# Kernel tuning notes

Hardware: AMD Instinct MI355X
Metric: run time of the kernel (lower is better)

Reference implementation:

```python
import jax, jax.numpy as jnp
import numpy as np

VOCAB = 32000
NUM_NEW = 512
HIDDEN = 4096
PROF_DIM = 64
MLP_HID = 256
B, S = 4, 4096


def setup_inputs() -> dict:
    key = jax.random.key(0)
    ks = jax.random.split(key, 8)
    return {
        "input_ids": jax.random.randint(ks[0], (B, S), 0, VOCAB + NUM_NEW),
        "emb_weight": jax.random.normal(ks[1], (VOCAB + NUM_NEW, HIDDEN), jnp.float32) * 0.02,
        "tool_semantics": jax.random.normal(ks[2], (NUM_NEW, HIDDEN), jnp.float32) * 0.02,
        "profiles": jax.random.normal(ks[3], (NUM_NEW, PROF_DIM), jnp.float32),
        "W1": jax.random.normal(ks[4], (PROF_DIM, MLP_HID), jnp.float32) * (1.0 / np.sqrt(PROF_DIM)),
        "b1": jnp.zeros((MLP_HID,), jnp.float32),
        "W2": jax.random.normal(ks[5], (MLP_HID, HIDDEN), jnp.float32) * (1.0 / np.sqrt(MLP_HID)),
        "b2": jnp.zeros((HIDDEN,), jnp.float32),
        "new_token_start_idx": VOCAB,
    }


def reference(input_ids, emb_weight, tool_semantics, profiles, W1, b1, W2, b2, new_token_start_idx):
    # Base embedding lookup: [B, S, H]
    base = emb_weight[input_ids]
    is_new = input_ids >= new_token_start_idx  # [B, S] bool
    # Clip relative indices so gathers are always in-range (masked out elsewhere)
    rel = jnp.clip(input_ids - new_token_start_idx, 0, tool_semantics.shape[0] - 1)
    sem = tool_semantics[rel]          # [B, S, H]
    prof = profiles[rel]               # [B, S, P]
    # Profile encoder MLP (hypernetwork): P -> MLP_HID -> H
    h = jax.nn.relu(jnp.einsum("bsp,ph->bsh", prof, W1) + b1)
    delta = jnp.einsum("bsh,hd->bsd", h, W2) + b2
    # Token_Embedding = semantics + profile delta for tool tokens, else base
    return jnp.where(is_new[..., None], sem + delta, base)
```

## Files before the change

### kernel.cpp

```cpp
#include <hip/hip_runtime.h>
#include <hip/hip_bf16.h>

constexpr int VOCAB    = 32000;
constexpr int NUM_NEW  = 512;
constexpr int HIDDEN   = 4096;
constexpr int PROF_DIM = 64;
constexpr int MLP_HID  = 256;

constexpr int TOK_PER_BLK  = 8;
constexpr int COLS_PER_BLK = 512;

typedef float f32x4 __attribute__((ext_vector_type(4)));

__global__ __launch_bounds__(256) void build_combined_kernel(
    const float* __restrict__ tool_semantics,
    const float* __restrict__ profiles,
    const float* __restrict__ W1,
    const float* __restrict__ b1,
    const float* __restrict__ W2,
    const float* __restrict__ b2,
    float* __restrict__ combined)
{
    __shared__ float prof_s[TOK_PER_BLK][PROF_DIM];
    __shared__ float h_s[TOK_PER_BLK][MLP_HID];

    const int t    = threadIdx.x;
    const int tok0 = blockIdx.y * TOK_PER_BLK;
    const int col0 = blockIdx.x * COLS_PER_BLK;

    for (int i = t; i < TOK_PER_BLK * PROF_DIM; i += 256) {
        const int tok = i / PROF_DIM;
        const int p   = i % PROF_DIM;
        prof_s[tok][p] = profiles[(tok0 + tok) * PROF_DIM + p];
    }
    __syncthreads();

    {
        float acc[TOK_PER_BLK];
        const float bias = b1[t];
#pragma unroll
        for (int tok = 0; tok < TOK_PER_BLK; ++tok) acc[tok] = bias;
        for (int p = 0; p < PROF_DIM; ++p) {
            const float w = W1[p * MLP_HID + t];
#pragma unroll
            for (int tok = 0; tok < TOK_PER_BLK; ++tok)
                acc[tok] = fmaf(prof_s[tok][p], w, acc[tok]);
        }
#pragma unroll
        for (int tok = 0; tok < TOK_PER_BLK; ++tok)
            h_s[tok][t] = fmaxf(acc[tok], 0.0f);
    }
    __syncthreads();

    const int c = col0 + t * 2;
    float2 acc2[TOK_PER_BLK];
#pragma unroll
    for (int tok = 0; tok < TOK_PER_BLK; ++tok) acc2[tok] = make_float2(0.f, 0.f);

    for (int k = 0; k < MLP_HID; ++k) {
        const float2 w2 = *(const float2*)&W2[k * HIDDEN + c];
#pragma unroll
        for (int tok = 0; tok < TOK_PER_BLK; ++tok) {
            const float hv = h_s[tok][k];
            acc2[tok].x = fmaf(hv, w2.x, acc2[tok].x);
            acc2[tok].y = fmaf(hv, w2.y, acc2[tok].y);
        }
    }

    const float2 bias2 = *(const float2*)&b2[c];
#pragma unroll
    for (int tok = 0; tok < TOK_PER_BLK; ++tok) {
        const float2 sem = *(const float2*)&tool_semantics[(size_t)(tok0 + tok) * HIDDEN + c];
        float2 r;
        r.x = sem.x + acc2[tok].x + bias2.x;
        r.y = sem.y + acc2[tok].y + bias2.y;
        *(float2*)&combined[(size_t)(tok0 + tok) * HIDDEN + c] = r;
    }
}

__global__ __launch_bounds__(256) void gather_rows_kernel(
    const int* __restrict__ input_ids,
    const float* __restrict__ emb_weight,
    const float* __restrict__ combined,
    const int* __restrict__ new_start_ptr,
    float* __restrict__ out)
{
    const int row       = blockIdx.x;
    const int id        = input_ids[row];
    const int new_start = *new_start_ptr;

    const float* src;
    if (id >= new_start) {
        int rel = id - new_start;
        if (rel > NUM_NEW - 1) rel = NUM_NEW - 1;
        src = combined + (size_t)rel * HIDDEN;
    } else {
        src = emb_weight + (size_t)id * HIDDEN;
    }

    const f32x4* s = (const f32x4*)src;
    f32x4*       d = (f32x4*)(out + (size_t)row * HIDDEN);
    const int t = threadIdx.x;

    f32x4 v0 = s[t];
    f32x4 v1 = s[t + 256];
    f32x4 v2 = s[t + 512];
    f32x4 v3 = s[t + 768];
    __builtin_nontemporal_store(v0, d + t);
    __builtin_nontemporal_store(v1, d + t + 256);
    __builtin_nontemporal_store(v2, d + t + 512);
    __builtin_nontemporal_store(v3, d + t + 768);
}

extern "C" void kernel_launch(void* const* d_in, const int* in_sizes, int n_in,
                              void* d_out, int out_size, void* d_ws, size_t ws_size,
                              hipStream_t stream) {
    const int*   input_ids      = (const int*)d_in[0];
    const float* emb_weight     = (const float*)d_in[1];
    const float* tool_semantics = (const float*)d_in[2];
    const float* profiles       = (const float*)d_in[3];
    const float* W1             = (const float*)d_in[4];
    const float* b1             = (const float*)d_in[5];
    const float* W2             = (const float*)d_in[6];
    const float* b2             = (const float*)d_in[7];
    const int*   new_start_ptr  = (const int*)d_in[8];
    float*       out            = (float*)d_out;

    const int num_rows = in_sizes[0];

    float* combined = (float*)d_ws;

    dim3 gridA(HIDDEN / COLS_PER_BLK, NUM_NEW / TOK_PER_BLK);
    build_combined_kernel<<<gridA, 256, 0, stream>>>(
        tool_semantics, profiles, W1, b1, W2, b2, combined);

    gather_rows_kernel<<<num_rows, 256, 0, stream>>>(
        input_ids, emb_weight, combined, new_start_ptr, out);
}
```

Measured before the change: 770.6 us.

## Fuse tool-token MLP into per-row gather, dropping precomputed combined table

Replaces the two-kernel scheme, which precomputed a 512-row combined table and then gathered from it, with a single kernel. Each row block either copies its base embedding row or runs the profile MLP for that one token. This removes a launch and the workspace round trip. In exchange, every tool token recomputes the full 256x4096 W2 product. With random ids about 1.6% of 16384 rows (~250 rows) are tool tokens, so W2 is read about 250 times instead of once per 8 tokens, and those blocks become long serial tails.

Result: slower. 821.2 us (+6.6%).

```diff
diff --git a/kernel.cpp b/kernel.cpp
--- a/kernel.cpp
+++ b/kernel.cpp
@@ -7,109 +7,84 @@
 constexpr int PROF_DIM = 64;
 constexpr int MLP_HID  = 256;
 
-constexpr int TOK_PER_BLK  = 8;
-constexpr int COLS_PER_BLK = 512;
-
 typedef float f32x4 __attribute__((ext_vector_type(4)));
 
-__global__ __launch_bounds__(256) void build_combined_kernel(
+__global__ __launch_bounds__(256) void fused_embed_kernel(
+    const int*   __restrict__ input_ids,
+    const float* __restrict__ emb_weight,
     const float* __restrict__ tool_semantics,
     const float* __restrict__ profiles,
     const float* __restrict__ W1,
     const float* __restrict__ b1,
     const float* __restrict__ W2,
     const float* __restrict__ b2,
-    float* __restrict__ combined)
+    const int*   __restrict__ new_start_ptr,
+    float*       __restrict__ out)
 {
-    __shared__ float prof_s[TOK_PER_BLK][PROF_DIM];
-    __shared__ float h_s[TOK_PER_BLK][MLP_HID];
+    __shared__ float prof_s[PROF_DIM];
+    __shared__ float h_s[MLP_HID];
 
-    const int t    = threadIdx.x;
-    const int tok0 = blockIdx.y * TOK_PER_BLK;
-    const int col0 = blockIdx.x * COLS_PER_BLK;
+    const int row       = blockIdx.x;
+    const int t         = threadIdx.x;
+    const int id        = input_ids[row];
+    const int new_start = *new_start_ptr;
 
-    for (int i = t; i < TOK_PER_BLK * PROF_DIM; i += 256) {
-        const int tok = i / PROF_DIM;
-        const int p   = i % PROF_DIM;
-        prof_s[tok][p] = profiles[(tok0 + tok) * PROF_DIM + p];
+    f32x4* d = (f32x4*)(out + (size_t)row * HIDDEN);
+
+    if (id < new_start) {
+        const f32x4* s = (const f32x4*)(emb_weight + (size_t)id * HIDDEN);
+        f32x4 v0 = s[t];
+        f32x4 v1 = s[t + 256];
+        f32x4 v2 = s[t + 512];
+        f32x4 v3 = s[t + 768];
+        __builtin_nontemporal_store(v0, d + t);
+        __builtin_nontemporal_store(v1, d + t + 256);
+        __builtin_nontemporal_store(v2, d + t + 512);
+        __builtin_nontemporal_store(v3, d + t + 768);
+        return;
+    }
+
+    int rel = id - new_start;
+    if (rel > NUM_NEW - 1) rel = NUM_NEW - 1;
+
+    if (t < PROF_DIM) prof_s[t] = profiles[rel * PROF_DIM + t];
+    __syncthreads();
+
+    {
+        float acc = b1[t];
+#pragma unroll
+        for (int p = 0; p < PROF_DIM; ++p)
+            acc = fmaf(prof_s[p], W1[p * MLP_HID + t], acc);
+        h_s[t] = fmaxf(acc, 0.0f);
     }
     __syncthreads();
 
-    {
-        float acc[TOK_PER_BLK];
-        const float bias = b1[t];
-#pragma unroll
-        for (int tok = 0; tok < TOK_PER_BLK; ++tok) acc[tok] = bias;
-        for (int p = 0; p < PROF_DIM; ++p) {
-            const float w = W1[p * MLP_HID + t];
-#pragma unroll
-            for (int tok = 0; tok < TOK_PER_BLK; ++tok)
-                acc[tok] = fmaf(prof_s[tok][p], w, acc[tok]);
-        }
-#pragma unroll
-        for (int tok = 0; tok < TOK_PER_BLK; ++tok)
-            h_s[tok][t] = fmaxf(acc[tok], 0.0f);
-    }
-    __syncthreads();
+    const f32x4* sem4 = (const f32x4*)(tool_semantics + (size_t)rel * HIDDEN);
+    const f32x4* b2_4 = (const f32x4*)b2;
+    const f32x4* W2_4 = (const f32x4*)W2;
 
-    const int c = col0 + t * 2;
-    float2 acc2[TOK_PER_BLK];
-#pragma unroll
-    for (int tok = 0; tok < TOK_PER_BLK; ++tok) acc2[tok] = make_float2(0.f, 0.f);
+    f32x4 acc0 = sem4[t]       + b2_4[t];
+    f32x4 acc1 = sem4[t + 256] + b2_4[t + 256];
+    f32x4 acc2 = sem4[t + 512] + b2_4[t + 512];
+    f32x4 acc3 = sem4[t + 768] + b2_4[t + 768];
 
     for (int k = 0; k < MLP_HID; ++k) {
-        const float2 w2 = *(const float2*)&W2[k * HIDDEN + c];
-#pragma unroll
-        for (int tok = 0; tok < TOK_PER_BLK; ++tok) {
-            const float hv = h_s[tok][k];
-            acc2[tok].x = fmaf(hv, w2.x, acc2[tok].x);
-            acc2[tok].y = fmaf(hv, w2.y, acc2[tok].y);
-        }
+        const float hv = h_s[k];
+        const f32x4* w2row = W2_4 + (size_t)k * (HIDDEN / 4);
+        const f32x4 w0 = w2row[t];
+        const f32x4 w1 = w2row[t + 256];
+        const f32x4 w2v = w2row[t + 512];
+        const f32x4 w3 = w2row[t + 768];
+        acc0 += hv * w0;
+        acc1 += hv * w1;
+        acc2 += hv * w2v;
+        acc3 += hv * w3;
     }
 
-    const float2 bias2 = *(const float2*)&b2[c];
-#pragma unroll
-    for (int tok = 0; tok < TOK_PER_BLK; ++tok) {
-        const float2 sem = *(const float2*)&tool_semantics[(size_t)(tok0 + tok) * HIDDEN + c];
-        float2 r;
-        r.x = sem.x + acc2[tok].x + bias2.x;
-        r.y = sem.y + acc2[tok].y + bias2.y;
-        *(float2*)&combined[(size_t)(tok0 + tok) * HIDDEN + c] = r;
-    }
-}
-
-__global__ __launch_bounds__(256) void gather_rows_kernel(
-    const int* __restrict__ input_ids,
-    const float* __restrict__ emb_weight,
-    const float* __restrict__ combined,
-    const int* __restrict__ new_start_ptr,
-    float* __restrict__ out)
-{
-    const int row       = blockIdx.x;
-    const int id        = input_ids[row];
-    const int new_start = *new_start_ptr;
-
-    const float* src;
-    if (id >= new_start) {
-        int rel = id - new_start;
-        if (rel > NUM_NEW - 1) rel = NUM_NEW - 1;
-        src = combined + (size_t)rel * HIDDEN;
-    } else {
-        src = emb_weight + (size_t)id * HIDDEN;
-    }
-
-    const f32x4* s = (const f32x4*)src;
-    f32x4*       d = (f32x4*)(out + (size_t)row * HIDDEN);
-    const int t = threadIdx.x;
-
-    f32x4 v0 = s[t];
-    f32x4 v1 = s[t + 256];
-    f32x4 v2 = s[t + 512];
-    f32x4 v3 = s[t + 768];
-    __builtin_nontemporal_store(v0, d + t);
-    __builtin_nontemporal_store(v1, d + t + 256);
-    __builtin_nontemporal_store(v2, d + t + 512);
-    __builtin_nontemporal_store(v3, d + t + 768);
+    __builtin_nontemporal_store(acc0, d + t);
+    __builtin_nontemporal_store(acc1, d + t + 256);
+    __builtin_nontemporal_store(acc2, d + t + 512);
+    __builtin_nontemporal_store(acc3, d + t + 768);
 }
 
 extern "C" void kernel_launch(void* const* d_in, const int* in_sizes, int n_in,
@@ -128,12 +103,7 @@
 
     const int num_rows = in_sizes[0];
 
-    float* combined = (float*)d_ws;
-
-    dim3 gridA(HIDDEN / COLS_PER_BLK, NUM_NEW / TOK_PER_BLK);
-    build_combined_kernel<<<gridA, 256, 0, stream>>>(
-        tool_semantics, profiles, W1, b1, W2, b2, combined);
-
-    gather_rows_kernel<<<num_rows, 256, 0, stream>>>(
-        input_ids, emb_weight, combined, new_start_ptr, out);
+    fused_embed_kernel<<<num_rows, 256, 0, stream>>>(
+        input_ids, emb_weight, tool_semantics, profiles,
+        W1, b1, W2, b2, new_start_ptr, out);
 }
```
